# Performance work log

Hardware: AMD Instinct MI355X
Metric: run time of the kernel (lower is better)

The kernel has to match this reference:

```python
import jax, jax.numpy as jnp
import numpy as np

B, N, C, K, H = 64, 4096, 256, 8, 256  # H = max(dim, hidden_dim=128)
ITERS = 3
EPS = 1e-8


def _ln(x, g, b):
    # torch LayerNorm: biased variance, eps=1e-5
    m = x.mean(-1, keepdims=True)
    v = ((x - m) ** 2).mean(-1, keepdims=True)
    return (x - m) * jax.lax.rsqrt(v + 1e-5) * g + b


def setup_inputs() -> dict:
    key = jax.random.key(0)
    ks = jax.random.split(key, 16)
    s = 0.02
    d = {}
    d['inputs'] = jax.random.normal(ks[0], (B, N, C), jnp.float32)
    d['slots_noise'] = jax.random.normal(ks[1], (K, C), jnp.float32)  # eval-mode shared noise
    d['mu'] = jax.random.normal(ks[2], (C,), jnp.float32)
    d['log_sigma'] = jax.random.normal(ks[3], (C,), jnp.float32) * 0.1
    d['ln_in_g'] = jnp.ones((C,), jnp.float32); d['ln_in_b'] = jnp.zeros((C,), jnp.float32)
    d['ln_s_g'] = jnp.ones((C,), jnp.float32); d['ln_s_b'] = jnp.zeros((C,), jnp.float32)
    d['ln_ff_g'] = jnp.ones((C,), jnp.float32); d['ln_ff_b'] = jnp.zeros((C,), jnp.float32)
    d['Wq'] = jax.random.normal(ks[4], (C, C), jnp.float32) * s; d['bq'] = jnp.zeros((C,), jnp.float32)
    d['Wk'] = jax.random.normal(ks[5], (C, C), jnp.float32) * s; d['bk'] = jnp.zeros((C,), jnp.float32)
    d['Wv'] = jax.random.normal(ks[6], (C, C), jnp.float32) * s; d['bv'] = jnp.zeros((C,), jnp.float32)
    d['W_ih'] = jax.random.normal(ks[7], (C, 3 * C), jnp.float32) * s; d['b_ih'] = jnp.zeros((3 * C,), jnp.float32)
    d['W_hh'] = jax.random.normal(ks[8], (C, 3 * C), jnp.float32) * s; d['b_hh'] = jnp.zeros((3 * C,), jnp.float32)
    d['W1'] = jax.random.normal(ks[9], (C, H), jnp.float32) * s; d['b1'] = jnp.zeros((H,), jnp.float32)
    d['W2'] = jax.random.normal(ks[10], (H, C), jnp.float32) * s; d['b2'] = jnp.zeros((C,), jnp.float32)
    return d


def reference(inputs, slots_noise, mu, log_sigma,
              ln_in_g, ln_in_b, ln_s_g, ln_s_b, ln_ff_g, ln_ff_b,
              Wq, bq, Wk, bk, Wv, bv,
              W_ih, b_ih, W_hh, b_hh,
              W1, b1, W2, b2):
    scale = C ** (-0.5)
    # eval-mode slot init: mu + exp(log_sigma) * noise, shared across batch
    slots = jnp.broadcast_to(mu + jnp.exp(log_sigma) * slots_noise, (B, K, C))
    x = _ln(inputs, ln_in_g, ln_in_b)
    k = x @ Wk + bk  # [B,N,C]
    v = x @ Wv + bv  # [B,N,C]
    for _ in range(ITERS):
        slots_prev = slots
        sn = _ln(slots, ln_s_g, ln_s_b)
        q = sn @ Wq + bq  # [B,K,C]
        dots = jnp.einsum('bid,bjd->bij', q, k) * scale  # [B,K,N]
        attn = jax.nn.softmax(dots, axis=1) + EPS  # softmax over slots (queries)
        attn = attn / attn.sum(-1, keepdims=True)  # renormalize over keys
        updates = jnp.einsum('bjd,bij->bid', v, attn)  # [B,K,C]
        # torch GRUCell
        gx = updates @ W_ih + b_ih
        gh = slots_prev @ W_hh + b_hh
        xr, xz, xn = jnp.split(gx, 3, axis=-1)
        hr, hz, hn = jnp.split(gh, 3, axis=-1)
        r = jax.nn.sigmoid(xr + hr)
        z = jax.nn.sigmoid(xz + hz)
        n = jnp.tanh(xn + r * hn)
        slots = (1.0 - z) * n + z * slots_prev
        pre = _ln(slots, ln_ff_g, ln_ff_b)
        slots = slots + (jax.nn.relu(pre @ W1 + b1) @ W2 + b2)
    return slots
```

## Files before the change

kernel.cpp:

```cpp
#include <hip/hip_runtime.h>
#include <hip/hip_bf16.h>

#define B_ 64
#define N_ 4096
#define C_ 256
#define K_ 8
#define M_ (B_*N_)
#define ITERS_ 3
#define SCALE_ 0.0625f
#define EPS_ 1e-8f

typedef __attribute__((ext_vector_type(4))) float f32x4;
typedef __attribute__((ext_vector_type(8))) __bf16 bf16x8;
typedef __attribute__((ext_vector_type(8))) unsigned short ushort8;
typedef __attribute__((ext_vector_type(4))) unsigned short ushort4v;

static __device__ __forceinline__ unsigned short f2bf(float f){
    union { float f; unsigned u; } v; v.f = f;
    unsigned r = v.u + 0x7fffu + ((v.u >> 16) & 1u);
    return (unsigned short)(r >> 16);
}
static __device__ __forceinline__ float bf2f(unsigned short h){
    union { unsigned u; float f; } v; v.u = ((unsigned)h) << 16;
    return v.f;
}

__global__ void prep1_kernel(const float* __restrict__ mu, const float* __restrict__ lsig,
                             const float* __restrict__ noise, float* __restrict__ slots){
    int idx = blockIdx.x*256 + threadIdx.x;
    int c = idx & 255, i = (idx >> 8) & 7;
    slots[idx] = mu[c] + expf(lsig[c])*noise[i*256 + c];
}

__global__ void prep2_kernel(const float* __restrict__ Wq, const float* __restrict__ Wk,
                             const float* __restrict__ bq, const float* __restrict__ bk,
                             float* __restrict__ WqkT, float* __restrict__ bqt,
                             float* __restrict__ wqb, float* __restrict__ bqkv){
    __shared__ float wqrow[256], bkl[256], bql[256];
    __shared__ float red[4], red2[4];
    const int t = threadIdx.x, c = blockIdx.x;
    wqrow[t] = Wq[(size_t)c*256 + t];
    bkl[t] = bk[t];
    bql[t] = bq[t];
    __syncthreads();
    float acc = 0.f, accb = 0.f;
    const float* wkr = Wk + (size_t)t*256;
    #pragma unroll 4
    for (int d = 0; d < 256; d += 4){
        float4 wk4 = *(const float4*)(wkr + d);
        float4 wq4 = *(const float4*)(&wqrow[d]);
        float4 bq4 = *(const float4*)(&bql[d]);
        acc  += wq4.x*wk4.x + wq4.y*wk4.y + wq4.z*wk4.z + wq4.w*wk4.w;
        accb += bq4.x*wk4.x + bq4.y*wk4.y + bq4.z*wk4.z + bq4.w*wk4.w;
    }
    WqkT[(size_t)c*256 + t] = acc;
    if (c == 0) bqt[t] = accb;
    float pw = wqrow[t]*bkl[t];
    float pb = bql[t]*bkl[t];
    #pragma unroll
    for (int m = 1; m < 64; m <<= 1){ pw += __shfl_xor(pw, m); pb += __shfl_xor(pb, m); }
    if ((t & 63) == 0){ red[t >> 6] = pw; red2[t >> 6] = pb; }
    __syncthreads();
    if (t == 0){
        wqb[c] = red[0] + red[1] + red[2] + red[3];
        if (c == 0) bqkv[0] = red2[0] + red2[1] + red2[2] + red2[3];
    }
}

__global__ void ln_kernel(const float* __restrict__ x, const float* __restrict__ g,
                          const float* __restrict__ bta, unsigned short* __restrict__ XH){
    const int t = threadIdx.x;
    const int row = blockIdx.x*32 + (t >> 3), s = t & 7;
    const float* xr = x + (size_t)row*C_;
    float v[32];
    #pragma unroll
    for (int q = 0; q < 8; ++q)
        *(float4*)&v[q*4] = *(const float4*)(xr + s*4 + q*32);
    float sum = 0.f, sq = 0.f;
    #pragma unroll
    for (int e = 0; e < 32; ++e){ sum += v[e]; sq += v[e]*v[e]; }
    #pragma unroll
    for (int m = 1; m < 8; m <<= 1){ sum += __shfl_xor(sum, m); sq += __shfl_xor(sq, m); }
    float mean = sum * (1.f/256.f);
    float rstd = rsqrtf(sq * (1.f/256.f) - mean*mean + 1e-5f);
    const int jt = row >> 8, rloc = row & 255;
    #pragma unroll
    for (int q = 0; q < 8; ++q){
        float4 g4 = *(const float4*)(g + q*32 + s*4);
        float4 b4 = *(const float4*)(bta + q*32 + s*4);
        ushort4v pk;
        pk[0] = f2bf((v[q*4+0] - mean)*rstd*g4.x + b4.x);
        pk[1] = f2bf((v[q*4+1] - mean)*rstd*g4.y + b4.y);
        pk[2] = f2bf((v[q*4+2] - mean)*rstd*g4.z + b4.z);
        pk[3] = f2bf((v[q*4+3] - mean)*rstd*g4.w + b4.w);
        *(ushort4v*)(XH + (((size_t)jt*8 + q)*256 + rloc)*32 + s*4) = pk;
    }
}

__global__ void slotq_kernel(const float* __restrict__ slots, const float* __restrict__ WqkT,
                             const float* __restrict__ bqt, const float* __restrict__ wqb,
                             const float* __restrict__ bqkv, const float* __restrict__ gs,
                             const float* __restrict__ bs, float* __restrict__ qtbuf,
                             float* __restrict__ qbb){
    __shared__ float sn[8][260];
    const int t = threadIdx.x, b = blockIdx.x, cgb = blockIdx.y;
    const int i = t >> 6, l = t & 63;
    {
        float4 v4 = *(const float4*)(slots + ((size_t)b*8 + i)*256 + l*4);
        float sum = v4.x + v4.y + v4.z + v4.w;
        float sq  = v4.x*v4.x + v4.y*v4.y + v4.z*v4.z + v4.w*v4.w;
        #pragma unroll
        for (int m = 1; m < 64; m <<= 1){ sum += __shfl_xor(sum, m); sq += __shfl_xor(sq, m); }
        float mean = sum * (1.f/256.f);
        float rstd = rsqrtf(sq * (1.f/256.f) - mean*mean + 1e-5f);
        float4 g4 = *(const float4*)(gs + l*4);
        float4 b4 = *(const float4*)(bs + l*4);
        float n0 = (v4.x - mean)*rstd*g4.x + b4.x;
        float n1 = (v4.y - mean)*rstd*g4.y + b4.y;
        float n2 = (v4.z - mean)*rstd*g4.z + b4.z;
        float n3 = (v4.w - mean)*rstd*g4.w + b4.w;
        sn[i][l*4+0] = n0; sn[i][l*4+1] = n1; sn[i][l*4+2] = n2; sn[i][l*4+3] = n3;
        if (cgb == 0){
            float4 w4 = *(const float4*)(wqb + l*4);
            float pb = n0*w4.x + n1*w4.y + n2*w4.z + n3*w4.w;
            #pragma unroll
            for (int m = 1; m < 64; m <<= 1) pb += __shfl_xor(pb, m);
            if (l == 0) qbb[(size_t)b*8 + i] = SCALE_*(pb + bqkv[0]);
        }
    }
    __syncthreads();
    const int col = cgb*64 + l;
    float acc = bqt[col];
    #pragma unroll
    for (int cb = 0; cb < 256; cb += 64){
        float w[64];
        #pragma unroll
        for (int u = 0; u < 64; ++u) w[u] = WqkT[(size_t)(cb+u)*256 + col];
        #pragma unroll
        for (int u = 0; u < 64; ++u) acc += sn[i][cb+u]*w[u];
    }
    qtbuf[((size_t)b*8 + i)*256 + col] = SCALE_*acc;
}

__global__ __launch_bounds__(512)
void attn_kernel(const unsigned short* __restrict__ XH, const float* __restrict__ qt,
                 const float* __restrict__ qb, float* __restrict__ Spart,
                 float* __restrict__ Upart){
    __shared__ __align__(16) unsigned short xs[4*8192];
    __shared__ __align__(16) unsigned short pst[2][16*40];
    __shared__ float swred[2][8];
    const int t = threadIdx.x, b = blockIdx.x, jb = blockIdx.y;
    const unsigned short* XB = XH + (size_t)(b*16 + jb)*65536;
    const int wv = t >> 6, l = t & 63;
    const int bi = l & 15, kg = l >> 4;
    const bool isQK = (wv < 2), isST = (wv == 2 || wv == 3), isPV = (wv >= 4);

    bf16x8 bfrag[8];
    float qbl = 0.f;
    {
        const ushort8 zz = (ushort8){0,0,0,0,0,0,0,0};
        #pragma unroll
        for (int ks = 0; ks < 8; ++ks) bfrag[ks] = __builtin_bit_cast(bf16x8, zz);
        if (isQK && bi < 8){
            #pragma unroll
            for (int ks = 0; ks < 8; ++ks){
                const float* qp = qt + ((size_t)b*8 + bi)*256 + ks*32 + kg*8;
                float4 qa = *(const float4*)qp;
                float4 qc = *(const float4*)(qp + 4);
                ushort8 pk;
                pk[0]=f2bf(qa.x); pk[1]=f2bf(qa.y); pk[2]=f2bf(qa.z); pk[3]=f2bf(qa.w);
                pk[4]=f2bf(qc.x); pk[5]=f2bf(qc.y); pk[6]=f2bf(qc.z); pk[7]=f2bf(qc.w);
                bfrag[ks] = __builtin_bit_cast(bf16x8, pk);
            }
            qbl = qb[(size_t)b*8 + bi];
        }
    }
    const int rstg = (wv & 1)*16 + (l >> 2);
    const int u4 = l & 3;
    const int swrr = (rstg & 7) ^ (((rstg >> 3) & 3) << 1);
    ushort8 S[8];
    f32x4 acc[4];
    #pragma unroll
    for (int n = 0; n < 4; ++n) acc[n] = (f32x4){0.f,0.f,0.f,0.f};
    const int pv_lo = bi & 7;
    const int pv_sl = (bi >> 3) ^ (kg << 1);
    float s8loc = 0.f;

#define STG_LOAD(ch) { \
    _Pragma("unroll") for (int og = 0; og < 8; ++og) \
        S[og] = *(const ushort8*)(XB + ((size_t)og*256 + (ch)*32 + rstg)*32 + u4*8); }
#define STG_WRITE(ch) { \
    unsigned short* xw = &xs[((ch)&3)*8192 + rstg*256]; \
    _Pragma("unroll") for (int og = 0; og < 8; ++og) \
        *(ushort8*)&xw[(((og*4 + u4) ^ swrr)*8)] = S[og]; }
#define BARR() { asm volatile("s_waitcnt lgkmcnt(0)" ::: "memory"); __builtin_amdgcn_s_barrier(); }

    if (isST){
        STG_LOAD(0); STG_WRITE(0);
        STG_LOAD(1);
    }
    BARR();

    #pragma unroll
    for (int p = 0; p < 8; ++p){
        if (isPV && p >= 1){
            const int cur = ((p-1) & 3) * 8192;
            ushort8 pa = *(const ushort8*)&pst[(p-1) & 1][bi*40 + kg*8];
            #pragma unroll
            for (int n = 0; n < 4; ++n){
                const int ct2 = ((wv - 4)*4 + n) << 1;
                ushort8 xv;
                #pragma unroll
                for (int e = 0; e < 8; ++e){
                    int slot = ct2 ^ pv_sl ^ e;
                    xv[e] = xs[cur + kg*2048 + e*256 + (slot << 3) + pv_lo];
                }
                acc[n] = __builtin_amdgcn_mfma_f32_16x16x32_bf16(
                    __builtin_bit_cast(bf16x8, pa), __builtin_bit_cast(bf16x8, xv), acc[n], 0, 0, 0);
            }
        }
        if (isQK){
            const int cur = (p & 3) * 8192;
            f32x4 qacc = (f32x4){0.f,0.f,0.f,0.f};
            const int rowL = wv*16 + bi;
            const int swrow = (rowL & 7) ^ (((rowL >> 3) & 3) << 1);
            const unsigned short* xrow = &xs[cur + rowL*256];
            #pragma unroll
            for (int ks = 0; ks < 8; ++ks){
                int chn = (ks*4 + kg) ^ swrow;
                bf16x8 af = *(const bf16x8*)&xrow[chn*8];
                qacc = __builtin_amdgcn_mfma_f32_16x16x32_bf16(af, bfrag[ks], qacc, 0, 0, 0);
            }
            ushort4v p4;
            #pragma unroll
            for (int rr = 0; rr < 4; ++rr){
                float d = qacc[rr] + qbl;
                float mx = d;
                mx = fmaxf(mx, __shfl_xor(mx, 1));
                mx = fmaxf(mx, __shfl_xor(mx, 2));
                mx = fmaxf(mx, __shfl_xor(mx, 4));
                float e = __expf(d - mx);
                float se = e;
                se += __shfl_xor(se, 1);
                se += __shfl_xor(se, 2);
                se += __shfl_xor(se, 4);
                float pv = e/se + EPS_;
                p4[rr] = f2bf(pv);
                if (bi < 8) s8loc += pv;
            }
            if (bi < 8)
                *(ushort4v*)&pst[p & 1][bi*40 + wv*16 + kg*4] = p4;
        }
        if (isST){
            if (p + 1 <= 7) STG_WRITE(p + 1);
            if (p + 2 <= 7) STG_LOAD(p + 2);
        }
        BARR();
    }
    if (isPV){
        const int cur = (7 & 3) * 8192;
        ushort8 pa = *(const ushort8*)&pst[7 & 1][bi*40 + kg*8];
        #pragma unroll
        for (int n = 0; n < 4; ++n){
            const int ct2 = ((wv - 4)*4 + n) << 1;
            ushort8 xv;
            #pragma unroll
            for (int e = 0; e < 8; ++e){
                int slot = ct2 ^ pv_sl ^ e;
                xv[e] = xs[cur + kg*2048 + e*256 + (slot << 3) + pv_lo];
            }
            acc[n] = __builtin_amdgcn_mfma_f32_16x16x32_bf16(
                __builtin_bit_cast(bf16x8, pa), __builtin_bit_cast(bf16x8, xv), acc[n], 0, 0, 0);
        }
    }
    if (isQK){
        float s = s8loc;
        s += __shfl_xor(s, 16);
        s += __shfl_xor(s, 32);
        if (l < 8) swred[wv][l] = s;
    }
    BARR();
    if (t < 8)
        Spart[((size_t)(b*16 + jb))*8 + t] = swred[0][t] + swred[1][t];
    if (isPV && kg < 2){
        #pragma unroll
        for (int n = 0; n < 4; ++n){
            const int ct = (wv - 4)*4 + n;
            #pragma unroll
            for (int r2 = 0; r2 < 4; ++r2){
                int i = kg*4 + r2;
                Upart[(((size_t)(b*16 + jb))*8 + i)*256 + ct*16 + bi] = acc[n][r2];
            }
        }
    }
#undef STG_LOAD
#undef STG_WRITE
#undef BARR
}

__global__ void slotu1_kernel(const float* __restrict__ slots, const float* __restrict__ Spart,
                              const float* __restrict__ Upart, const float* __restrict__ Wv,
                              const float* __restrict__ bv, const float* __restrict__ W_ih,
                              const float* __restrict__ b_ih, const float* __restrict__ W_hh,
                              const float* __restrict__ b_hh, float* __restrict__ slots2){
    __shared__ float us[8][260], sp[8][260], upd[8][260];
    const int t = threadIdx.x, b = blockIdx.x, ng = blockIdx.y;
    const int i = t >> 6, l = t & 63;
    {
        float a0 = 0.f, a1 = 0.f, a2 = 0.f, a3 = 0.f, S = 0.f;
        #pragma unroll
        for (int jbl = 0; jbl < 16; ++jbl){
            float4 u4 = *(const float4*)(Upart + (((size_t)(b*16 + jbl))*8 + i)*256 + l*4);
            a0 += u4.x; a1 += u4.y; a2 += u4.z; a3 += u4.w;
            S += Spart[((size_t)(b*16 + jbl))*8 + i];
        }
        float invS = 1.f / S;
        us[i][l*4+0] = a0*invS; us[i][l*4+1] = a1*invS;
        us[i][l*4+2] = a2*invS; us[i][l*4+3] = a3*invS;
        float4 s4 = *(const float4*)(slots + ((size_t)b*8 + i)*256 + l*4);
        sp[i][l*4+0] = s4.x; sp[i][l*4+1] = s4.y; sp[i][l*4+2] = s4.z; sp[i][l*4+3] = s4.w;
    }
    __syncthreads();
    {
        const int c4 = l*4;
        float4 acc = *(const float4*)(bv + c4);
        #pragma unroll
        for (int cb = 0; cb < 256; cb += 16){
            float4 w4[16];
            #pragma unroll
            for (int u = 0; u < 16; ++u)
                w4[u] = *(const float4*)(Wv + (size_t)(cb+u)*256 + c4);
            #pragma unroll
            for (int u = 0; u < 16; ++u){
                float uv = us[i][cb+u];
                acc.x += uv*w4[u].x; acc.y += uv*w4[u].y;
                acc.z += uv*w4[u].z; acc.w += uv*w4[u].w;
            }
        }
        *(float4*)&upd[i][c4] = acc;
    }
    __syncthreads();
    {
        const int n = ng*64 + l;
        float xr = b_ih[n], xz = b_ih[256+n], xn = b_ih[512+n];
        float hr = b_hh[n], hz = b_hh[256+n], hn = b_hh[512+n];
        #pragma unroll 2
        for (int cb = 0; cb < 256; cb += 8){
            float wi0[8], wi1[8], wi2[8], wh0[8], wh1[8], wh2[8];
            #pragma unroll
            for (int u = 0; u < 8; ++u){
                const float* wi = W_ih + (size_t)(cb+u)*768 + n;
                const float* wh = W_hh + (size_t)(cb+u)*768 + n;
                wi0[u] = wi[0]; wi1[u] = wi[256]; wi2[u] = wi[512];
                wh0[u] = wh[0]; wh1[u] = wh[256]; wh2[u] = wh[512];
            }
            #pragma unroll
            for (int u = 0; u < 8; ++u){
                float uv = upd[i][cb+u], sv = sp[i][cb+u];
                xr += uv*wi0[u]; xz += uv*wi1[u]; xn += uv*wi2[u];
                hr += sv*wh0[u]; hz += sv*wh1[u]; hn += sv*wh2[u];
            }
        }
        float rv = 1.f/(1.f + __expf(-(xr + hr)));
        float zv = 1.f/(1.f + __expf(-(xz + hz)));
        float nn = tanhf(xn + rv*hn);
        slots2[((size_t)b*8 + i)*256 + n] = (1.f - zv)*nn + zv*sp[i][n];
    }
}

__global__ void slotu2_kernel(const float* __restrict__ slots2, const float* __restrict__ gf,
                              const float* __restrict__ bf, const float* __restrict__ W1,
                              const float* __restrict__ b1, const float* __restrict__ W2,
                              const float* __restrict__ b2, float* __restrict__ slots,
                              float* __restrict__ dout){
    __shared__ float s0[8][260], pre[8][260], hb[8][260];
    const int t = threadIdx.x, b = blockIdx.x, ng = blockIdx.y;
    const int i = t >> 6, l = t & 63;
    {
        float4 v4 = *(const float4*)(slots2 + ((size_t)b*8 + i)*256 + l*4);
        float sum = v4.x + v4.y + v4.z + v4.w;
        float sq  = v4.x*v4.x + v4.y*v4.y + v4.z*v4.z + v4.w*v4.w;
        #pragma unroll
        for (int m = 1; m < 64; m <<= 1){ sum += __shfl_xor(sum, m); sq += __shfl_xor(sq, m); }
        float mean = sum * (1.f/256.f);
        float rstd = rsqrtf(sq * (1.f/256.f) - mean*mean + 1e-5f);
        float4 g4 = *(const float4*)(gf + l*4);
        float4 b4 = *(const float4*)(bf + l*4);
        s0[i][l*4+0] = v4.x; s0[i][l*4+1] = v4.y; s0[i][l*4+2] = v4.z; s0[i][l*4+3] = v4.w;
        pre[i][l*4+0] = (v4.x - mean)*rstd*g4.x + b4.x;
        pre[i][l*4+1] = (v4.y - mean)*rstd*g4.y + b4.y;
        pre[i][l*4+2] = (v4.z - mean)*rstd*g4.z + b4.z;
        pre[i][l*4+3] = (v4.w - mean)*rstd*g4.w + b4.w;
    }
    __syncthreads();
    {
        const int h4 = l*4;
        float4 acc = *(const float4*)(b1 + h4);
        #pragma unroll
        for (int cb = 0; cb < 256; cb += 16){
            float4 w4[16];
            #pragma unroll
            for (int u = 0; u < 16; ++u)
                w4[u] = *(const float4*)(W1 + (size_t)(cb+u)*256 + h4);
            #pragma unroll
            for (int u = 0; u < 16; ++u){
                float pv = pre[i][cb+u];
                acc.x += pv*w4[u].x; acc.y += pv*w4[u].y;
                acc.z += pv*w4[u].z; acc.w += pv*w4[u].w;
            }
        }
        hb[i][h4+0] = fmaxf(acc.x, 0.f); hb[i][h4+1] = fmaxf(acc.y, 0.f);
        hb[i][h4+2] = fmaxf(acc.z, 0.f); hb[i][h4+3] = fmaxf(acc.w, 0.f);
    }
    __syncthreads();
    {
        const int n = ng*64 + l;
        float acc = b2[n];
        #pragma unroll
        for (int mb = 0; mb < 256; mb += 64){
            float w[64];
            #pragma unroll
            for (int u = 0; u < 64; ++u) w[u] = W2[(size_t)(mb+u)*256 + n];
            #pragma unroll
            for (int u = 0; u < 64; ++u) acc += hb[i][mb+u]*w[u];
        }
        float val = s0[i][n] + acc;
        size_t off = ((size_t)b*8 + i)*256 + n;
        slots[off] = val;
        dout[off]  = val;
    }
}

extern "C" void kernel_launch(void* const* d_in, const int* in_sizes, int n_in,
                              void* d_out, int out_size, void* d_ws, size_t ws_size,
                              hipStream_t stream){
    const float* inputs = (const float*)d_in[0];
    const float* noise  = (const float*)d_in[1];
    const float* mu     = (const float*)d_in[2];
    const float* lsig   = (const float*)d_in[3];
    const float* g_in   = (const float*)d_in[4];
    const float* b_in   = (const float*)d_in[5];
    const float* g_s    = (const float*)d_in[6];
    const float* b_s    = (const float*)d_in[7];
    const float* g_ff   = (const float*)d_in[8];
    const float* b_ff   = (const float*)d_in[9];
    const float* Wq     = (const float*)d_in[10];
    const float* bq     = (const float*)d_in[11];
    const float* Wk     = (const float*)d_in[12];
    const float* bk     = (const float*)d_in[13];
    const float* Wv     = (const float*)d_in[14];
    const float* bv     = (const float*)d_in[15];
    const float* W_ih   = (const float*)d_in[16];
    const float* b_ih   = (const float*)d_in[17];
    const float* W_hh   = (const float*)d_in[18];
    const float* b_hh   = (const float*)d_in[19];
    const float* W1     = (const float*)d_in[20];
    const float* b1     = (const float*)d_in[21];
    const float* W2     = (const float*)d_in[22];
    const float* b2     = (const float*)d_in[23];

    char* ws = (char*)d_ws;
    unsigned short* XH  = (unsigned short*)(ws);
    float* Upart        = (float*)(ws + ((size_t)128 << 20));
    float* Spart        = (float*)(ws + ((size_t)136 << 20));
    float* qtbuf        = (float*)(ws + ((size_t)137 << 20));
    float* qbb          = (float*)(ws + ((size_t)138 << 20));
    float* slots        = (float*)(ws + ((size_t)139 << 20));
    float* slots2       = (float*)(ws + ((size_t)140 << 20));
    float* WqkT         = (float*)(ws + ((size_t)141 << 20));
    float* bqt          = (float*)(ws + ((size_t)142 << 20));
    float* wqb          = (float*)(ws + ((size_t)143 << 20));
    float* bqkv         = (float*)(ws + ((size_t)144 << 20));

    prep1_kernel<<<512, 256, 0, stream>>>(mu, lsig, noise, slots);
    prep2_kernel<<<256, 256, 0, stream>>>(Wq, Wk, bq, bk, WqkT, bqt, wqb, bqkv);
    ln_kernel<<<M_/32, 256, 0, stream>>>(inputs, g_in, b_in, XH);
    for (int it = 0; it < ITERS_; ++it){
        slotq_kernel<<<dim3(B_, 4), 512, 0, stream>>>(slots, WqkT, bqt, wqb, bqkv,
                                                      g_s, b_s, qtbuf, qbb);
        attn_kernel<<<dim3(B_, 16), 512, 0, stream>>>(XH, qtbuf, qbb, Spart, Upart);
        slotu1_kernel<<<dim3(B_, 4), 512, 0, stream>>>(slots, Spart, Upart, Wv, bv,
                                                       W_ih, b_ih, W_hh, b_hh, slots2);
        slotu2_kernel<<<dim3(B_, 4), 512, 0, stream>>>(slots2, g_ff, b_ff, W1, b1, W2, b2,
                                                       slots, (float*)d_out);
    }
}
```

Baseline: 459.4 us.

## Restructure attention kernel pipeline: four QK waves, all waves stage, 64-row chunks

Moves the attention kernel from eight 32-row phases with two dedicated staging waves to four 64-row phases. In the new scheme all eight waves issue global loads into double-buffered LDS, and four waves do QK/softmax instead of two. PV waves now run two MFMA k-halves per phase, and the P buffer is widened to 64 columns. The aim is fewer barriers per tile and more wave-level parallelism on the QK and staging paths. The cost is more barriers per phase (QK and PV are now serialized within each phase) and a larger register footprint for two staging buffers.

Result: slower. 473.1 us (+3.0%).

```diff
diff --git a/kernel.cpp b/kernel.cpp
--- a/kernel.cpp
+++ b/kernel.cpp
@@ -146,14 +146,14 @@
 void attn_kernel(const unsigned short* __restrict__ XH, const float* __restrict__ qt,
                  const float* __restrict__ qb, float* __restrict__ Spart,
                  float* __restrict__ Upart){
-    __shared__ __align__(16) unsigned short xs[4*8192];
-    __shared__ __align__(16) unsigned short pst[2][16*40];
-    __shared__ float swred[2][8];
+    __shared__ __align__(16) unsigned short xs[2*16384];
+    __shared__ __align__(16) unsigned short pst[16*72];
+    __shared__ float swred[4][8];
     const int t = threadIdx.x, b = blockIdx.x, jb = blockIdx.y;
     const unsigned short* XB = XH + (size_t)(b*16 + jb)*65536;
     const int wv = t >> 6, l = t & 63;
     const int bi = l & 15, kg = l >> 4;
-    const bool isQK = (wv < 2), isST = (wv == 2 || wv == 3), isPV = (wv >= 4);
+    const bool isQK = (wv < 4), isPV = (wv >= 4);
 
     bf16x8 bfrag[8];
     float qbl = 0.f;
@@ -175,10 +175,8 @@
             qbl = qb[(size_t)b*8 + bi];
         }
     }
-    const int rstg = (wv & 1)*16 + (l >> 2);
-    const int u4 = l & 3;
-    const int swrr = (rstg & 7) ^ (((rstg >> 3) & 3) << 1);
-    ushort8 S[8];
+    ushort8 SbA[4], SbB[4];
+    const int strow[4] = { (l >> 2), 16 + (l >> 2), 32 + (l >> 2), 48 + (l >> 2) };
     f32x4 acc[4];
     #pragma unroll
     for (int n = 0; n < 4; ++n) acc[n] = (f32x4){0.f,0.f,0.f,0.f};
@@ -186,93 +184,82 @@
     const int pv_sl = (bi >> 3) ^ (kg << 1);
     float s8loc = 0.f;
 
-#define STG_LOAD(ch) { \
-    _Pragma("unroll") for (int og = 0; og < 8; ++og) \
-        S[og] = *(const ushort8*)(XB + ((size_t)og*256 + (ch)*32 + rstg)*32 + u4*8); }
-#define STG_WRITE(ch) { \
-    unsigned short* xw = &xs[((ch)&3)*8192 + rstg*256]; \
-    _Pragma("unroll") for (int og = 0; og < 8; ++og) \
-        *(ushort8*)&xw[(((og*4 + u4) ^ swrr)*8)] = S[og]; }
+#define STG_LOAD(Sb, ch) { \
+    const unsigned short* gp = XB + (size_t)wv*8192 + (ch)*2048 + l*8; \
+    _Pragma("unroll") for (int u = 0; u < 4; ++u) Sb[u] = *(const ushort8*)(gp + u*512); }
+#define STG_WRITE(Sb, ch) { \
+    unsigned short* xw = &xs[((ch)&1)*16384]; \
+    _Pragma("unroll") for (int u = 0; u < 4; ++u){ \
+        int rr = strow[u]; \
+        int o = (wv*4 + (l & 3)) ^ ((rr & 7) ^ (((rr >> 3) & 3) << 1)); \
+        *(ushort8*)&xw[rr*256 + o*8] = Sb[u]; } }
 #define BARR() { asm volatile("s_waitcnt lgkmcnt(0)" ::: "memory"); __builtin_amdgcn_s_barrier(); }
 
-    if (isST){
-        STG_LOAD(0); STG_WRITE(0);
-        STG_LOAD(1);
-    }
-    BARR();
-
-    #pragma unroll
-    for (int p = 0; p < 8; ++p){
-        if (isPV && p >= 1){
-            const int cur = ((p-1) & 3) * 8192;
-            ushort8 pa = *(const ushort8*)&pst[(p-1) & 1][bi*40 + kg*8];
-            #pragma unroll
-            for (int n = 0; n < 4; ++n){
-                const int ct2 = ((wv - 4)*4 + n) << 1;
-                ushort8 xv;
-                #pragma unroll
-                for (int e = 0; e < 8; ++e){
-                    int slot = ct2 ^ pv_sl ^ e;
-                    xv[e] = xs[cur + kg*2048 + e*256 + (slot << 3) + pv_lo];
-                }
-                acc[n] = __builtin_amdgcn_mfma_f32_16x16x32_bf16(
-                    __builtin_bit_cast(bf16x8, pa), __builtin_bit_cast(bf16x8, xv), acc[n], 0, 0, 0);
-            }
-        }
-        if (isQK){
-            const int cur = (p & 3) * 8192;
-            f32x4 qacc = (f32x4){0.f,0.f,0.f,0.f};
-            const int rowL = wv*16 + bi;
-            const int swrow = (rowL & 7) ^ (((rowL >> 3) & 3) << 1);
-            const unsigned short* xrow = &xs[cur + rowL*256];
-            #pragma unroll
-            for (int ks = 0; ks < 8; ++ks){
-                int chn = (ks*4 + kg) ^ swrow;
-                bf16x8 af = *(const bf16x8*)&xrow[chn*8];
-                qacc = __builtin_amdgcn_mfma_f32_16x16x32_bf16(af, bfrag[ks], qacc, 0, 0, 0);
-            }
-            ushort4v p4;
-            #pragma unroll
-            for (int rr = 0; rr < 4; ++rr){
-                float d = qacc[rr] + qbl;
-                float mx = d;
-                mx = fmaxf(mx, __shfl_xor(mx, 1));
-                mx = fmaxf(mx, __shfl_xor(mx, 2));
-                mx = fmaxf(mx, __shfl_xor(mx, 4));
-                float e = __expf(d - mx);
-                float se = e;
-                se += __shfl_xor(se, 1);
-                se += __shfl_xor(se, 2);
-                se += __shfl_xor(se, 4);
-                float pv = e/se + EPS_;
-                p4[rr] = f2bf(pv);
-                if (bi < 8) s8loc += pv;
-            }
-            if (bi < 8)
-                *(ushort4v*)&pst[p & 1][bi*40 + wv*16 + kg*4] = p4;
-        }
-        if (isST){
-            if (p + 1 <= 7) STG_WRITE(p + 1);
-            if (p + 2 <= 7) STG_LOAD(p + 2);
-        }
-        BARR();
-    }
-    if (isPV){
-        const int cur = (7 & 3) * 8192;
-        ushort8 pa = *(const ushort8*)&pst[7 & 1][bi*40 + kg*8];
-        #pragma unroll
-        for (int n = 0; n < 4; ++n){
-            const int ct2 = ((wv - 4)*4 + n) << 1;
-            ushort8 xv;
-            #pragma unroll
-            for (int e = 0; e < 8; ++e){
-                int slot = ct2 ^ pv_sl ^ e;
-                xv[e] = xs[cur + kg*2048 + e*256 + (slot << 3) + pv_lo];
-            }
-            acc[n] = __builtin_amdgcn_mfma_f32_16x16x32_bf16(
-                __builtin_bit_cast(bf16x8, pa), __builtin_bit_cast(bf16x8, xv), acc[n], 0, 0, 0);
-        }
-    }
+#define QK_PHASE(p) if (isQK){ \
+    const int cur = ((p)&1)*16384; \
+    f32x4 qacc = (f32x4){0.f,0.f,0.f,0.f}; \
+    const int rowL = wv*16 + bi; \
+    const int swrow = (rowL & 7) ^ (((rowL >> 3) & 3) << 1); \
+    const unsigned short* xrow = &xs[cur + rowL*256]; \
+    _Pragma("unroll") for (int ks = 0; ks < 8; ++ks){ \
+        int chn = (ks*4 + kg) ^ swrow; \
+        bf16x8 af = *(const bf16x8*)&xrow[chn*8]; \
+        qacc = __builtin_amdgcn_mfma_f32_16x16x32_bf16(af, bfrag[ks], qacc, 0, 0, 0); } \
+    ushort4v p4; \
+    _Pragma("unroll") for (int rr = 0; rr < 4; ++rr){ \
+        float d = qacc[rr] + qbl; \
+        float mx = d; \
+        mx = fmaxf(mx, __shfl_xor(mx, 1)); \
+        mx = fmaxf(mx, __shfl_xor(mx, 2)); \
+        mx = fmaxf(mx, __shfl_xor(mx, 4)); \
+        float e = __expf(d - mx); \
+        float se = e; \
+        se += __shfl_xor(se, 1); \
+        se += __shfl_xor(se, 2); \
+        se += __shfl_xor(se, 4); \
+        float pv = e/se + EPS_; \
+        p4[rr] = f2bf(pv); \
+        if (bi < 8) s8loc += pv; } \
+    if (bi < 8) *(ushort4v*)&pst[bi*72 + wv*16 + kg*4] = p4; }
+
+#define PV_PHASE(p) if (isPV){ \
+    const int cur = ((p)&1)*16384; \
+    _Pragma("unroll") for (int kh = 0; kh < 2; ++kh){ \
+        ushort8 pa = *(const ushort8*)&pst[bi*72 + kh*32 + kg*8]; \
+        _Pragma("unroll") for (int n = 0; n < 4; ++n){ \
+            const int ct2 = ((wv - 4)*4 + n) << 1; \
+            ushort8 xv; \
+            _Pragma("unroll") for (int e = 0; e < 8; ++e){ \
+                int slot = ct2 ^ pv_sl ^ e; \
+                xv[e] = xs[cur + kh*8192 + kg*2048 + e*256 + (slot << 3) + pv_lo]; } \
+            acc[n] = __builtin_amdgcn_mfma_f32_16x16x32_bf16( \
+                __builtin_bit_cast(bf16x8, pa), __builtin_bit_cast(bf16x8, xv), acc[n], 0, 0, 0); } } }
+
+    STG_LOAD(SbA, 0); STG_WRITE(SbA, 0);
+    STG_LOAD(SbB, 1);
+    BARR();
+
+    STG_LOAD(SbA, 2);
+    QK_PHASE(0)
+    BARR();
+    PV_PHASE(0)
+    STG_WRITE(SbB, 1);
+    BARR();
+    STG_LOAD(SbB, 3);
+    QK_PHASE(1)
+    BARR();
+    PV_PHASE(1)
+    STG_WRITE(SbA, 2);
+    BARR();
+    QK_PHASE(2)
+    BARR();
+    PV_PHASE(2)
+    STG_WRITE(SbB, 3);
+    BARR();
+    QK_PHASE(3)
+    BARR();
+    PV_PHASE(3)
+
     if (isQK){
         float s = s8loc;
         s += __shfl_xor(s, 16);
@@ -281,7 +268,8 @@
     }
     BARR();
     if (t < 8)
-        Spart[((size_t)(b*16 + jb))*8 + t] = swred[0][t] + swred[1][t];
+        Spart[((size_t)(b*16 + jb))*8 + t] =
+            swred[0][t] + swred[1][t] + swred[2][t] + swred[3][t];
     if (isPV && kg < 2){
         #pragma unroll
         for (int n = 0; n < 4; ++n){
@@ -296,6 +284,8 @@
 #undef STG_LOAD
 #undef STG_WRITE
 #undef BARR
+#undef QK_PHASE
+#undef PV_PHASE
 }
 
 __global__ void slotu1_kernel(const float* __restrict__ slots, const float* __restrict__ Spart,
```
